# Optimization experiments

Hardware: AMD Instinct MI355X
Metric: run time of the kernel (lower is better)

## Reference

```python
import jax, jax.numpy as jnp
import numpy as np

N = 50000
E = 1600000
D = 128
H = 16  # SE hidden = int(128 * 0.125)
EPS = 1e-5


def _layernorm(x, gamma, beta):
    mu = jnp.mean(x, axis=-1, keepdims=True)
    var = jnp.mean(jnp.square(x - mu), axis=-1, keepdims=True)
    return (x - mu) * jax.lax.rsqrt(var + EPS) * gamma + beta


def _gcn_conv(x, W, b, src, dst):
    # PyG GCNConv, improved=True: self-loop weight 2.0, symmetric norm.
    xw = x @ W                                        # [N, D]
    deg = jax.ops.segment_sum(jnp.ones((E,), x.dtype), dst, num_segments=N) + 2.0
    dinv = jnp.where(deg > 0, jax.lax.rsqrt(deg), 0.0)  # [N]
    norm = dinv[src] * dinv[dst]                      # [E]
    agg = jax.ops.segment_sum(xw[src] * norm[:, None], dst, num_segments=N)
    agg = agg + xw * (2.0 * dinv * dinv)[:, None]     # self-loop contribution
    return agg + b


def setup_inputs() -> dict:
    key = jax.random.key(0)
    ks = jax.random.split(key, 10)
    scale = 1.0 / np.sqrt(D)
    inp = {
        "x": jax.random.normal(ks[0], (N, D), jnp.float32),
        "edge_index": jax.random.randint(ks[1], (2, E), 0, N, jnp.int64),
        "W1": jax.random.normal(ks[2], (D, D), jnp.float32) * scale,
        "b1": jnp.zeros((D,), jnp.float32),
        "g1": jnp.ones((D,), jnp.float32),
        "beta1": jnp.zeros((D,), jnp.float32),
        "W2": jax.random.normal(ks[3], (D, D), jnp.float32) * scale,
        "b2": jnp.zeros((D,), jnp.float32),
        "g2": jnp.ones((D,), jnp.float32),
        "beta2": jnp.zeros((D,), jnp.float32),
        "Ws": jax.random.normal(ks[4], (D, H), jnp.float32) * scale,
        "bs": jnp.zeros((H,), jnp.float32),
        "We": jax.random.normal(ks[5], (H, D), jnp.float32) * (1.0 / np.sqrt(H)),
        "be": jnp.zeros((D,), jnp.float32),
    }
    return inp


def reference(x, edge_index, W1, b1, g1, beta1, W2, b2, g2, beta2, Ws, bs, We, be):
    src, dst = edge_index[0], edge_index[1]
    skip = x
    h = jax.nn.relu(_layernorm(_gcn_conv(x, W1, b1, src, dst), g1, beta1))
    h = _layernorm(_gcn_conv(h, W2, b2, src, dst), g2, beta2)
    # SE gating
    s = jax.nn.relu(h @ Ws + bs)
    w = jax.nn.sigmoid(s @ We + be)
    h = h * w
    return jax.nn.relu(h + skip)
```

## Files before the change

kernel.cpp:

```cpp
#include <hip/hip_runtime.h>
#include <math.h>

#define DD 128
#define HH 16
#define NB 256
#define TILE 8192
#define SEGCAP 24576
#define EPSV 1e-5f

typedef unsigned long long u64;

static __device__ __forceinline__ ushort f2bf(float f) {
  uint u = __float_as_uint(f);
  u += 0x7FFFu + ((u >> 16) & 1u);
  return (ushort)(u >> 16);
}
static __device__ __forceinline__ float bflo(uint u) { return __uint_as_float(u << 16); }
static __device__ __forceinline__ float bfhi(uint u) { return __uint_as_float(u & 0xFFFF0000u); }


__global__ void k_hist(const int* __restrict__ dst, int* __restrict__ deg, int ecnt) {
  int stride = gridDim.x * blockDim.x;
  for (int e = blockIdx.x * blockDim.x + threadIdx.x; e < ecnt; e += stride)
    atomicAdd(&deg[dst[e]], 1);
}


#define SCAN_T 1024
#define SCAN_I 4

__global__ void k_scan1(const int* __restrict__ deg, u64* __restrict__ bsum, int n) {
  __shared__ u64 sh[SCAN_T];
  int tid = threadIdx.x;
  int base = blockIdx.x * SCAN_T * SCAN_I + tid * SCAN_I;
  u64 s = 0;
#pragma unroll
  for (int j = 0; j < SCAN_I; ++j) {
    int i = base + j;
    if (i < n) {
      int d = deg[i];
      int dp = (d + 7) & ~7;
      s += ((u64)dp << 32) | (u64)(uint)d;
    }
  }
  sh[tid] = s;
  __syncthreads();
  for (int off = SCAN_T / 2; off > 0; off >>= 1) {
    if (tid < off) sh[tid] += sh[tid + off];
    __syncthreads();
  }
  if (tid == 0) bsum[blockIdx.x] = sh[0];
}

__global__ void k_scan2(const int* __restrict__ deg, const u64* __restrict__ bsum,
                        int* __restrict__ rowoff, int* __restrict__ cursor,
                        int* __restrict__ bucketBase, int* __restrict__ bucketCur,
                        int n) {
  __shared__ u64 sh[SCAN_T];
  __shared__ u64 sbase;
  int tid = threadIdx.x;
  int b = blockIdx.x;
  if (tid == 0) { u64 s = 0; for (int j = 0; j < b; ++j) s += bsum[j]; sbase = s; }
  int base = b * SCAN_T * SCAN_I + tid * SCAN_I;
  int d[SCAN_I]; u64 ts = 0;
#pragma unroll
  for (int j = 0; j < SCAN_I; ++j) {
    int i = base + j;
    d[j] = (i < n) ? deg[i] : 0;
    int dp = (d[j] + 7) & ~7;
    ts += ((u64)dp << 32) | (u64)(uint)d[j];
  }
  sh[tid] = ts;
  __syncthreads();
  for (int off = 1; off < SCAN_T; off <<= 1) {
    u64 v = (tid >= off) ? sh[tid - off] : 0;
    __syncthreads();
    sh[tid] += v;
    __syncthreads();
  }
  u64 ex = sbase + sh[tid] - ts;
#pragma unroll
  for (int j = 0; j < SCAN_I; ++j) {
    int i = base + j;
    if (i < n) {
      int ro = (int)(ex >> 32);
      int raw = (int)(ex & 0xFFFFFFFFu);
      rowoff[i] = ro;
      cursor[i] = ro;
      int bq = (int)(((uint)i * NB) / (uint)n);
      if (i == (bq * n + NB - 1) / NB) { bucketBase[bq] = raw; bucketCur[bq] = raw; }
      int dp = (d[j] + 7) & ~7;
      ex += ((u64)dp << 32) | (u64)(uint)d[j];
      if (i == n - 1) rowoff[n] = (int)(ex >> 32);
    }
  }
}


static __device__ __forceinline__ void gemm_f32_body(
    const float* __restrict__ A, const float* __restrict__ B,
    const int* __restrict__ deg, ushort* __restrict__ C, int nrows, int bx,
    float* Bs) {
  int tid = threadIdx.x;
  int tx = tid & 15, ty = tid >> 4;
  int rowbase = (bx >> 1) * 128;
  int c0 = (bx & 1) * 64;
  {
    int kk = tid >> 4;
    int cc = (tid & 15) * 4;
#pragma unroll
    for (int p = 0; p < 8; ++p) {
      int k = p * 16 + kk;
      float4 bv = *reinterpret_cast<const float4*>(&B[k * DD + c0 + cc]);
      *reinterpret_cast<float4*>(&Bs[k * 64 + cc]) = bv;
    }
  }
  __syncthreads();
  float acc[8][4];
#pragma unroll
  for (int i = 0; i < 8; ++i)
#pragma unroll
    for (int j = 0; j < 4; ++j) acc[i][j] = 0.f;
  int rl[8];
#pragma unroll
  for (int i = 0; i < 8; ++i) {
    int r = rowbase + ty * 8 + i;
    rl[i] = (r < nrows) ? r : (nrows - 1);
  }
  const float4* A4 = reinterpret_cast<const float4*>(A);
  for (int kq = 0; kq < 32; ++kq) {
    float4 av[8];
#pragma unroll
    for (int i = 0; i < 8; ++i) av[i] = A4[(size_t)rl[i] * 32 + kq];
#pragma unroll
    for (int j = 0; j < 4; ++j) {
      float4 bv = *reinterpret_cast<const float4*>(&Bs[(kq * 4 + j) * 64 + tx * 4]);
#pragma unroll
      for (int i = 0; i < 8; ++i) {
        float a = (j == 0) ? av[i].x : (j == 1) ? av[i].y : (j == 2) ? av[i].z : av[i].w;
        acc[i][0] = fmaf(a, bv.x, acc[i][0]);
        acc[i][1] = fmaf(a, bv.y, acc[i][1]);
        acc[i][2] = fmaf(a, bv.z, acc[i][2]);
        acc[i][3] = fmaf(a, bv.w, acc[i][3]);
      }
    }
  }
  int cbase = c0 + tx * 4;
#pragma unroll
  for (int i = 0; i < 8; ++i) {
    int r = rowbase + ty * 8 + i;
    if (r < nrows) {
      float dv = rsqrtf((float)deg[r] + 2.0f);
      ushort4 o;
      o.x = f2bf(acc[i][0] * dv); o.y = f2bf(acc[i][1] * dv);
      o.z = f2bf(acc[i][2] * dv); o.w = f2bf(acc[i][3] * dv);
      *reinterpret_cast<ushort4*>(&C[(size_t)r * DD + cbase]) = o;
    }
  }
}


__global__ __launch_bounds__(256) void k_gemm1_bucket(
    const float* __restrict__ A, const float* __restrict__ B,
    const int* __restrict__ deg, ushort* __restrict__ C, int nrows,
    const int* __restrict__ src, const int* __restrict__ dst,
    int* __restrict__ bucketCur, uint* __restrict__ pairs, int ecnt,
    int abloks, int gblocks) {
  __shared__ uint smem[8960];
  int bx = blockIdx.x;
  if (bx >= abloks) {
    gemm_f32_body(A, B, deg, C, nrows, bx - abloks, (float*)smem);
    return;
  }
  uint* stag  = smem;
  uint* cnt   = smem + 8192;
  uint* gbase = smem + 8448;
  uint* cur   = smem + 8704;
  int tid = threadIdx.x;
  int ntiles = (ecnt + TILE - 1) / TILE;
  for (int t = bx; t < ntiles; t += abloks) {
    int base = t * TILE;
    int cntE = min(TILE, ecnt - base);
    cnt[tid] = 0;
    __syncthreads();
    for (int k = tid; k < cntE; k += 256) {
      uint d = (uint)dst[base + k];
      atomicAdd(&cnt[(d * NB) / (uint)nrows], 1u);
    }
    __syncthreads();
    uint myc = cnt[tid];
    uint gb = atomicAdd((uint*)&bucketCur[tid], myc);
    uint v = myc;
#pragma unroll
    for (int off = 1; off < 64; off <<= 1) {
      uint u = __shfl_up(v, off, 64);
      if ((tid & 63) >= off) v += u;
    }
    if ((tid & 63) == 63) gbase[tid >> 6] = v;
    __syncthreads();
    uint add = 0;
#pragma unroll
    for (int wvi = 0; wvi < 4; ++wvi) add += (wvi < (tid >> 6)) ? gbase[wvi] : 0;
    uint excl = add + v - myc;
    __syncthreads();
    cnt[tid] = excl;
    gbase[tid] = gb;
    cur[tid] = 0;
    __syncthreads();
    for (int k = tid; k < cntE; k += 256) {
      uint d = (uint)dst[base + k];
      uint s = (uint)src[base + k];
      uint b = (d * NB) / (uint)nrows;
      uint li = atomicAdd(&cur[b], 1u);
      stag[cnt[b] + li] = (d << 16) | s;
    }
    __syncthreads();
    int wv = tid >> 6, ln = tid & 63;
    for (int b = wv; b < 256; b += 4) {
      uint c = cur[b], o = cnt[b], g = gbase[b];
      for (uint k2 = (uint)ln; k2 < c; k2 += 64) pairs[g + k2] = stag[o + k2];
    }
    __syncthreads();
  }
}


__global__ __launch_bounds__(256) void k_csrb(
    const uint* __restrict__ pairs, const int* __restrict__ bucketBase,
    const int* __restrict__ rowoff, const int* __restrict__ deg,
    int* __restrict__ cursor, ushort* __restrict__ csr, int n, int ecnt) {
  __shared__ ushort seg[SEGCAP];
  __shared__ int curs[256];
  int b = blockIdx.x;
  int tid = threadIdx.x;
  int d0 = (b * n + NB - 1) / NB;
  int d1 = ((b + 1) * n + NB - 1) / NB;
  int segbase = rowoff[d0];
  int seglen = rowoff[d1] - segbase;
  int pbase = bucketBase[b];
  int pend = (b == NB - 1) ? ecnt : bucketBase[b + 1];
  if (seglen <= SEGCAP) {
    for (int dl = tid; dl < d1 - d0; dl += 256) curs[dl] = rowoff[d0 + dl] - segbase;
    __syncthreads();
    for (int p = pbase + tid; p < pend; p += 256) {
      uint pr = pairs[p];
      int pos = atomicAdd(&curs[(int)(pr >> 16) - d0], 1);
      seg[pos] = (ushort)(pr & 0xFFFFu);
    }
    __syncthreads();
    for (int dl = tid; dl < d1 - d0; dl += 256) {
      int e0 = curs[dl], e1 = rowoff[d0 + dl + 1] - segbase;
      for (int k = e0; k < e1; ++k) seg[k] = (ushort)n;
    }
    __syncthreads();
    uint4* outp4 = (uint4*)(csr + segbase);
    const uint4* sp = (const uint4*)seg;
    int nq = seglen >> 3;
    for (int k = tid; k < nq; k += 256) outp4[k] = sp[k];
  } else {
    for (int p = pbase + tid; p < pend; p += 256) {
      uint pr = pairs[p];
      int pos = atomicAdd(&cursor[pr >> 16], 1);
      csr[pos] = (ushort)(pr & 0xFFFFu);
    }
    __syncthreads();
    for (int dl = tid; dl < d1 - d0; dl += 256) {
      int d = d0 + dl;
      for (int k = rowoff[d] + deg[d]; k < rowoff[d + 1]; ++k) csr[k] = (ushort)n;
    }
  }
}


__global__ __launch_bounds__(256) void k_gemmb(const ushort* __restrict__ A,
                                               const float* __restrict__ B,
                                               const int* __restrict__ deg,
                                               ushort* __restrict__ C, int nrows) {
  __shared__ float Bs[DD * 64];
  int tid = threadIdx.x;
  int tx = tid & 15, ty = tid >> 4;
  int rowbase = (blockIdx.x >> 1) * 128;
  int c0 = (blockIdx.x & 1) * 64;
  {
    int kk = tid >> 4;
    int cc = (tid & 15) * 4;
#pragma unroll
    for (int p = 0; p < 8; ++p) {
      int k = p * 16 + kk;
      float4 bv = *reinterpret_cast<const float4*>(&B[k * DD + c0 + cc]);
      *reinterpret_cast<float4*>(&Bs[k * 64 + cc]) = bv;
    }
  }
  __syncthreads();
  float acc[8][4];
#pragma unroll
  for (int i = 0; i < 8; ++i)
#pragma unroll
    for (int j = 0; j < 4; ++j) acc[i][j] = 0.f;
  int rl[8];
#pragma unroll
  for (int i = 0; i < 8; ++i) {
    int r = rowbase + ty * 8 + i;
    rl[i] = (r < nrows) ? r : (nrows - 1);
  }
  const uint4* A16 = reinterpret_cast<const uint4*>(A);
  for (int kq = 0; kq < 16; ++kq) {
    uint4 av[8];
#pragma unroll
    for (int i = 0; i < 8; ++i) av[i] = A16[(size_t)rl[i] * 16 + kq];
#pragma unroll
    for (int kk = 0; kk < 8; ++kk) {
      float4 bv = *reinterpret_cast<const float4*>(&Bs[(kq * 8 + kk) * 64 + tx * 4]);
#pragma unroll
      for (int i = 0; i < 8; ++i) {
        uint wq = (kk < 2) ? av[i].x : (kk < 4) ? av[i].y : (kk < 6) ? av[i].z : av[i].w;
        float a = (kk & 1) ? bfhi(wq) : bflo(wq);
        acc[i][0] = fmaf(a, bv.x, acc[i][0]);
        acc[i][1] = fmaf(a, bv.y, acc[i][1]);
        acc[i][2] = fmaf(a, bv.z, acc[i][2]);
        acc[i][3] = fmaf(a, bv.w, acc[i][3]);
      }
    }
  }
  int cbase = c0 + tx * 4;
#pragma unroll
  for (int i = 0; i < 8; ++i) {
    int r = rowbase + ty * 8 + i;
    if (r < nrows) {
      float dv = rsqrtf((float)deg[r] + 2.0f);
      ushort4 o;
      o.x = f2bf(acc[i][0] * dv); o.y = f2bf(acc[i][1] * dv);
      o.z = f2bf(acc[i][2] * dv); o.w = f2bf(acc[i][3] * dv);
      *reinterpret_cast<ushort4*>(&C[(size_t)r * DD + cbase]) = o;
    }
  }
}


static __device__ __forceinline__ void edge_accum(
    const uint* __restrict__ xw32, const ushort* __restrict__ csr,
    int start, int cnt, uint lane, float& acc0, float& acc1) {
  const uint4* cs = (const uint4*)(csr + __builtin_amdgcn_readfirstlane(start));
  int rem = __builtin_amdgcn_readfirstlane(cnt);
  uint4 c;
  if (rem >= 8) c = *cs++;
  while (rem >= 16) {
    uint v[8];
    v[0] = xw32[((c.x & 0xFFFFu) << 6) + lane];
    v[1] = xw32[((c.x >> 16) << 6) + lane];
    v[2] = xw32[((c.y & 0xFFFFu) << 6) + lane];
    v[3] = xw32[((c.y >> 16) << 6) + lane];
    v[4] = xw32[((c.z & 0xFFFFu) << 6) + lane];
    v[5] = xw32[((c.z >> 16) << 6) + lane];
    v[6] = xw32[((c.w & 0xFFFFu) << 6) + lane];
    v[7] = xw32[((c.w >> 16) << 6) + lane];
    uint4 cn = *cs++;
#pragma unroll
    for (int j = 0; j < 8; ++j) {
      acc0 += bflo(v[j]);
      acc1 += bfhi(v[j]);
    }
    c = cn; rem -= 8;
  }
  if (rem >= 8) {
    uint v[8];
    v[0] = xw32[((c.x & 0xFFFFu) << 6) + lane];
    v[1] = xw32[((c.x >> 16) << 6) + lane];
    v[2] = xw32[((c.y & 0xFFFFu) << 6) + lane];
    v[3] = xw32[((c.y >> 16) << 6) + lane];
    v[4] = xw32[((c.z & 0xFFFFu) << 6) + lane];
    v[5] = xw32[((c.z >> 16) << 6) + lane];
    v[6] = xw32[((c.w & 0xFFFFu) << 6) + lane];
    v[7] = xw32[((c.w >> 16) << 6) + lane];
#pragma unroll
    for (int j = 0; j < 8; ++j) {
      acc0 += bflo(v[j]);
      acc1 += bfhi(v[j]);
    }
  }
}


__global__ __launch_bounds__(256) void k_agg1(
    const ushort* __restrict__ xwd, const ushort* __restrict__ csr,
    const int* __restrict__ rowoff, const int* __restrict__ deg,
    const float* __restrict__ bias, const float* __restrict__ gam,
    const float* __restrict__ bet, uint* __restrict__ outp, int n) {
  int wv = threadIdx.x >> 6, lane = threadIdx.x & 63;
  int i = blockIdx.x * 4 + wv;
  if (i >= n) return;
  int start = rowoff[i], cnt = rowoff[i + 1] - start;
  float di = rsqrtf((float)deg[i] + 2.0f);
  const uint* xw32 = (const uint*)xwd;
  float acc0 = 0.f, acc1 = 0.f;
  edge_accum(xw32, csr, start, cnt, (uint)lane, acc0, acc1);
  uint su = xw32[((uint)i << 6) + lane];
  float2 bv = ((const float2*)bias)[lane];
  float c0v = fmaf(di, acc0 + 2.f * bflo(su), bv.x);
  float c1v = fmaf(di, acc1 + 2.f * bfhi(su), bv.y);
  float s = c0v + c1v;
#pragma unroll
  for (int off = 32; off > 0; off >>= 1) s += __shfl_xor(s, off);
  float mu = s * (1.f / DD);
  float c0 = c0v - mu, c1 = c1v - mu;
  float q = c0 * c0 + c1 * c1;
#pragma unroll
  for (int off = 32; off > 0; off >>= 1) q += __shfl_xor(q, off);
  float rstd = rsqrtf(q * (1.f / DD) + EPSV);
  float2 gv = ((const float2*)gam)[lane];
  float2 tv = ((const float2*)bet)[lane];
  float h0 = fmaxf(fmaf(c0 * rstd, gv.x, tv.x), 0.f);
  float h1 = fmaxf(fmaf(c1 * rstd, gv.y, tv.y), 0.f);
  uint packed = (uint)f2bf(h0) | ((uint)f2bf(h1) << 16);
  __builtin_nontemporal_store(packed, &outp[((uint)i << 6) + lane]);
}


__global__ __launch_bounds__(256) void k_agg2(
    const ushort* __restrict__ xwd, const ushort* __restrict__ csr,
    const int* __restrict__ rowoff, const int* __restrict__ deg,
    const float* __restrict__ bias, const float* __restrict__ gam,
    const float* __restrict__ bet, const float* __restrict__ Ws,
    const float* __restrict__ bs, const float* __restrict__ We,
    const float* __restrict__ be, const float* __restrict__ xin,
    float* __restrict__ outp, int n) {
  int wv = threadIdx.x >> 6, lane = threadIdx.x & 63;
  int i = blockIdx.x * 4 + wv;
  if (i >= n) return;
  int start = rowoff[i], cnt = rowoff[i + 1] - start;
  float di = rsqrtf((float)deg[i] + 2.0f);
  const uint* xw32 = (const uint*)xwd;
  float acc0 = 0.f, acc1 = 0.f;
  edge_accum(xw32, csr, start, cnt, (uint)lane, acc0, acc1);
  uint su = xw32[((uint)i << 6) + lane];
  float2 bv = ((const float2*)bias)[lane];
  float c0v = fmaf(di, acc0 + 2.f * bflo(su), bv.x);
  float c1v = fmaf(di, acc1 + 2.f * bfhi(su), bv.y);
  float s = c0v + c1v;
#pragma unroll
  for (int off = 32; off > 0; off >>= 1) s += __shfl_xor(s, off);
  float mu = s * (1.f / DD);
  float c0 = c0v - mu, c1 = c1v - mu;
  float q = c0 * c0 + c1 * c1;
#pragma unroll
  for (int off = 32; off > 0; off >>= 1) q += __shfl_xor(q, off);
  float rstd = rsqrtf(q * (1.f / DD) + EPSV);
  float2 gv = ((const float2*)gam)[lane];
  float2 tv = ((const float2*)bet)[lane];
  float h0 = fmaf(c0 * rstd, gv.x, tv.x);
  float h1 = fmaf(c1 * rstd, gv.y, tv.y);
  float pj[HH];
  const float* wr0 = &Ws[(2 * lane) * HH];
  const float* wr1 = &Ws[(2 * lane + 1) * HH];
#pragma unroll
  for (int j = 0; j < HH; ++j) pj[j] = h0 * wr0[j] + h1 * wr1[j];
#pragma unroll
  for (int off = 32; off > 0; off >>= 1) {
#pragma unroll
    for (int j = 0; j < HH; ++j) pj[j] += __shfl_xor(pj[j], off);
  }
  float2 bev = ((const float2*)be)[lane];
  float wacc0 = bev.x, wacc1 = bev.y;
#pragma unroll
  for (int j = 0; j < HH; ++j) {
    float sj = fmaxf(pj[j] + bs[j], 0.f);
    float2 wev = ((const float2*)(We + j * DD))[lane];
    wacc0 = fmaf(sj, wev.x, wacc0);
    wacc1 = fmaf(sj, wev.y, wacc1);
  }
  float w0 = 1.f / (1.f + __expf(-wacc0));
  float w1 = 1.f / (1.f + __expf(-wacc1));
  float2 xr = ((const float2*)(xin + (size_t)i * DD))[lane];
  float2 o;
  o.x = fmaxf(fmaf(h0, w0, xr.x), 0.f);
  o.y = fmaxf(fmaf(h1, w1, xr.y), 0.f);
  ((float2*)(outp + (size_t)i * DD))[lane] = o;
}


extern "C" void kernel_launch(void* const* d_in, const int* in_sizes, int n_in,
                              void* d_out, int out_size, void* d_ws, size_t ws_size,
                              hipStream_t stream) {
  const float* x   = (const float*)d_in[0];
  const int*   ei  = (const int*)d_in[1];
  const float* W1  = (const float*)d_in[2];
  const float* b1  = (const float*)d_in[3];
  const float* g1  = (const float*)d_in[4];
  const float* be1 = (const float*)d_in[5];
  const float* W2  = (const float*)d_in[6];
  const float* b2  = (const float*)d_in[7];
  const float* g2  = (const float*)d_in[8];
  const float* be2 = (const float*)d_in[9];
  const float* Ws  = (const float*)d_in[10];
  const float* bs  = (const float*)d_in[11];
  const float* We  = (const float*)d_in[12];
  const float* bee = (const float*)d_in[13];
  float* outp = (float*)d_out;

  int n    = in_sizes[0] / DD;
  int ecnt = in_sizes[1] / 2;
  const int* src = ei;
  const int* dst = ei + ecnt;

  size_t maxent = (size_t)ecnt + 8 * (size_t)n + 64;

  char* w = (char*)d_ws;
  ushort* xwd    = (ushort*)w; w += (size_t)(n + 1) * DD * 2;
  uint*   h1     = (uint*)w;   w += (size_t)n * DD * 2;
  int*    deg    = (int*)w;    w += (size_t)n * 4;
  int*    cursor = (int*)w;    w += (size_t)n * 4;
  int*    rowoff = (int*)w;    w += (size_t)(n + 1) * 4;
  w = (char*)(((size_t)w + 7) & ~(size_t)7);
  u64*    bsum   = (u64*)w;    w += 64 * 8;
  int*    bktB   = (int*)w;    w += NB * 4;
  int*    bktC   = (int*)w;    w += NB * 4;
  w = (char*)(((size_t)w + 15) & ~(size_t)15);
  uint*   pairs  = (uint*)w;   w += ((size_t)ecnt + 64) * 4;
  w = (char*)(((size_t)w + 15) & ~(size_t)15);
  ushort* csr    = (ushort*)w; w += maxent * 2;

  hipMemsetAsync(deg, 0, (size_t)n * 4, stream);
  hipMemsetAsync(xwd + (size_t)n * DD, 0, DD * 2, stream);

  const int TB = 256;
  k_hist<<<2048, TB, 0, stream>>>(dst, deg, ecnt);
  int nb = (n + SCAN_T * SCAN_I - 1) / (SCAN_T * SCAN_I);
  k_scan1<<<nb, SCAN_T, 0, stream>>>(deg, bsum, n);
  k_scan2<<<nb, SCAN_T, 0, stream>>>(deg, bsum, rowoff, cursor, bktB, bktC, n);

  int gblocks = ((n + 127) / 128) * 2;
  int abloks = (ecnt + TILE - 1) / TILE;
  k_gemm1_bucket<<<abloks + gblocks, TB, 0, stream>>>(
      x, W1, deg, xwd, n, src, dst, bktC, pairs, ecnt, abloks, gblocks);
  k_csrb<<<NB, TB, 0, stream>>>(pairs, bktB, rowoff, deg, cursor, csr, n, ecnt);

  int nb4 = (n + 3) / 4;
  k_agg1<<<nb4, TB, 0, stream>>>(xwd, csr, rowoff, deg, b1, g1, be1, h1, n);
  k_gemmb<<<gblocks, TB, 0, stream>>>((const ushort*)h1, W2, deg, xwd, n);
  k_agg2<<<nb4, TB, 0, stream>>>(xwd, csr, rowoff, deg, b2, g2, be2,
                                 Ws, bs, We, bee, x, outp, n);
}
```

Before: 326.7 us.

## Use bf16 MFMA for both dense GEMMs, pre-converting x to bf16 in histogram

Replaces the FP32 scalar-FMA GEMM bodies for XW1 and H1·W2 with a bf16 MFMA 16x16x32 kernel. Each wave loads its B fragments straight from global memory and converts them to bf16, with no LDS staging. The input x is converted to bf16 inside the degree-histogram kernel so the first GEMM can read packed bf16 rows, which costs an extra workspace buffer and a pass over x. This lowers first-layer GEMM precision to bf16 inputs, and output stores become 2-byte scattered writes per lane rather than vectorized.

Result: faster. 310.9 us (-4.8%).

```diff
diff --git a/kernel.cpp b/kernel.cpp
--- a/kernel.cpp
+++ b/kernel.cpp
@@ -9,6 +9,9 @@
 #define EPSV 1e-5f
 
 typedef unsigned long long u64;
+typedef __attribute__((ext_vector_type(8))) short short8;
+typedef __attribute__((ext_vector_type(4))) float f32x4;
+union U4S8 { uint4 u; short8 s; };
 
 static __device__ __forceinline__ ushort f2bf(float f) {
   uint u = __float_as_uint(f);
@@ -19,10 +22,16 @@
 static __device__ __forceinline__ float bfhi(uint u) { return __uint_as_float(u & 0xFFFF0000u); }
 
 
-__global__ void k_hist(const int* __restrict__ dst, int* __restrict__ deg, int ecnt) {
+__global__ void k_hist_cvt(const int* __restrict__ dst, int* __restrict__ deg, int ecnt,
+                           const float2* __restrict__ x2, uint* __restrict__ xb,
+                           int ncnt) {
   int stride = gridDim.x * blockDim.x;
-  for (int e = blockIdx.x * blockDim.x + threadIdx.x; e < ecnt; e += stride)
-    atomicAdd(&deg[dst[e]], 1);
+  int t0 = blockIdx.x * blockDim.x + threadIdx.x;
+  for (int e = t0; e < ecnt; e += stride) atomicAdd(&deg[dst[e]], 1);
+  for (int k = t0; k < ncnt; k += stride) {
+    float2 v = x2[k];
+    xb[k] = (uint)f2bf(v.x) | ((uint)f2bf(v.y) << 16);
+  }
 }
 
 
@@ -97,71 +106,52 @@
 }
 
 
-static __device__ __forceinline__ void gemm_f32_body(
-    const float* __restrict__ A, const float* __restrict__ B,
-    const int* __restrict__ deg, ushort* __restrict__ C, int nrows, int bx,
-    float* Bs) {
+static __device__ __forceinline__ void gemm_mfma_body(
+    const uint4* __restrict__ A16, const float* __restrict__ B,
+    const int* __restrict__ deg, ushort* __restrict__ C, int nrows, int bx) {
   int tid = threadIdx.x;
-  int tx = tid & 15, ty = tid >> 4;
-  int rowbase = (bx >> 1) * 128;
+  int wv = tid >> 6, l = tid & 63;
+  int rowbase = (bx >> 1) * 64;
   int c0 = (bx & 1) * 64;
-  {
-    int kk = tid >> 4;
-    int cc = (tid & 15) * 4;
-#pragma unroll
-    for (int p = 0; p < 8; ++p) {
-      int k = p * 16 + kk;
-      float4 bv = *reinterpret_cast<const float4*>(&B[k * DD + c0 + cc]);
-      *reinterpret_cast<float4*>(&Bs[k * 64 + cc]) = bv;
-    }
-  }
-  __syncthreads();
-  float acc[8][4];
-#pragma unroll
-  for (int i = 0; i < 8; ++i)
-#pragma unroll
-    for (int j = 0; j < 4; ++j) acc[i][j] = 0.f;
-  int rl[8];
-#pragma unroll
-  for (int i = 0; i < 8; ++i) {
-    int r = rowbase + ty * 8 + i;
-    rl[i] = (r < nrows) ? r : (nrows - 1);
-  }
-  const float4* A4 = reinterpret_cast<const float4*>(A);
-  for (int kq = 0; kq < 32; ++kq) {
-    float4 av[8];
-#pragma unroll
-    for (int i = 0; i < 8; ++i) av[i] = A4[(size_t)rl[i] * 32 + kq];
-#pragma unroll
-    for (int j = 0; j < 4; ++j) {
-      float4 bv = *reinterpret_cast<const float4*>(&Bs[(kq * 4 + j) * 64 + tx * 4]);
-#pragma unroll
-      for (int i = 0; i < 8; ++i) {
-        float a = (j == 0) ? av[i].x : (j == 1) ? av[i].y : (j == 2) ? av[i].z : av[i].w;
-        acc[i][0] = fmaf(a, bv.x, acc[i][0]);
-        acc[i][1] = fmaf(a, bv.y, acc[i][1]);
-        acc[i][2] = fmaf(a, bv.z, acc[i][2]);
-        acc[i][3] = fmaf(a, bv.w, acc[i][3]);
+  int colb = c0 + (wv << 4) + (l & 15);
+  int kb = (l >> 4) << 3;
+  uint4 bf[4];
+#pragma unroll
+  for (int ks = 0; ks < 4; ++ks) {
+    const float* Bp = B + (size_t)(ks * 32 + kb) * DD + colb;
+    float b0 = Bp[0], b1 = Bp[DD], b2 = Bp[2 * DD], b3 = Bp[3 * DD];
+    float b4 = Bp[4 * DD], b5 = Bp[5 * DD], b6 = Bp[6 * DD], b7 = Bp[7 * DD];
+    bf[ks].x = (uint)f2bf(b0) | ((uint)f2bf(b1) << 16);
+    bf[ks].y = (uint)f2bf(b2) | ((uint)f2bf(b3) << 16);
+    bf[ks].z = (uint)f2bf(b4) | ((uint)f2bf(b5) << 16);
+    bf[ks].w = (uint)f2bf(b6) | ((uint)f2bf(b7) << 16);
+  }
+#pragma unroll
+  for (int rt = 0; rt < 4; ++rt) {
+    int r = rowbase + rt * 16 + (l & 15);
+    int rc = (r < nrows) ? r : (nrows - 1);
+    f32x4 acc = {0.f, 0.f, 0.f, 0.f};
+#pragma unroll
+    for (int ks = 0; ks < 4; ++ks) {
+      U4S8 ua, ub;
+      ua.u = A16[(size_t)rc * 16 + (ks << 2) + (l >> 4)];
+      ub.u = bf[ks];
+      acc = __builtin_amdgcn_mfma_f32_16x16x32_bf16(ua.s, ub.s, acc, 0, 0, 0);
+    }
+#pragma unroll
+    for (int ri = 0; ri < 4; ++ri) {
+      int row = rowbase + rt * 16 + ((l >> 4) << 2) + ri;
+      if (row < nrows) {
+        float dv = rsqrtf((float)deg[row] + 2.0f);
+        C[(size_t)row * DD + colb] = f2bf(acc[ri] * dv);
       }
     }
   }
-  int cbase = c0 + tx * 4;
-#pragma unroll
-  for (int i = 0; i < 8; ++i) {
-    int r = rowbase + ty * 8 + i;
-    if (r < nrows) {
-      float dv = rsqrtf((float)deg[r] + 2.0f);
-      ushort4 o;
-      o.x = f2bf(acc[i][0] * dv); o.y = f2bf(acc[i][1] * dv);
-      o.z = f2bf(acc[i][2] * dv); o.w = f2bf(acc[i][3] * dv);
-      *reinterpret_cast<ushort4*>(&C[(size_t)r * DD + cbase]) = o;
-    }
-  }
 }
 
 
 __global__ __launch_bounds__(256) void k_gemm1_bucket(
-    const float* __restrict__ A, const float* __restrict__ B,
+    const uint4* __restrict__ A16, const float* __restrict__ B,
     const int* __restrict__ deg, ushort* __restrict__ C, int nrows,
     const int* __restrict__ src, const int* __restrict__ dst,
     int* __restrict__ bucketCur, uint* __restrict__ pairs, int ecnt,
@@ -169,7 +159,7 @@
   __shared__ uint smem[8960];
   int bx = blockIdx.x;
   if (bx >= abloks) {
-    gemm_f32_body(A, B, deg, C, nrows, bx - abloks, (float*)smem);
+    gemm_mfma_body(A16, B, deg, C, nrows, bx - abloks);
     return;
   }
   uint* stag  = smem;
@@ -222,6 +212,12 @@
     }
     __syncthreads();
   }
+}
+
+__global__ __launch_bounds__(256) void k_gemmb(
+    const uint4* __restrict__ A16, const float* __restrict__ B,
+    const int* __restrict__ deg, ushort* __restrict__ C, int nrows) {
+  gemm_mfma_body(A16, B, deg, C, nrows, blockIdx.x);
 }
 
 
@@ -267,71 +263,6 @@
     for (int dl = tid; dl < d1 - d0; dl += 256) {
       int d = d0 + dl;
       for (int k = rowoff[d] + deg[d]; k < rowoff[d + 1]; ++k) csr[k] = (ushort)n;
-    }
-  }
-}
-
-
-__global__ __launch_bounds__(256) void k_gemmb(const ushort* __restrict__ A,
-                                               const float* __restrict__ B,
-                                               const int* __restrict__ deg,
-                                               ushort* __restrict__ C, int nrows) {
-  __shared__ float Bs[DD * 64];
-  int tid = threadIdx.x;
-  int tx = tid & 15, ty = tid >> 4;
-  int rowbase = (blockIdx.x >> 1) * 128;
-  int c0 = (blockIdx.x & 1) * 64;
-  {
-    int kk = tid >> 4;
-    int cc = (tid & 15) * 4;
-#pragma unroll
-    for (int p = 0; p < 8; ++p) {
-      int k = p * 16 + kk;
-      float4 bv = *reinterpret_cast<const float4*>(&B[k * DD + c0 + cc]);
-      *reinterpret_cast<float4*>(&Bs[k * 64 + cc]) = bv;
-    }
-  }
-  __syncthreads();
-  float acc[8][4];
-#pragma unroll
-  for (int i = 0; i < 8; ++i)
-#pragma unroll
-    for (int j = 0; j < 4; ++j) acc[i][j] = 0.f;
-  int rl[8];
-#pragma unroll
-  for (int i = 0; i < 8; ++i) {
-    int r = rowbase + ty * 8 + i;
-    rl[i] = (r < nrows) ? r : (nrows - 1);
-  }
-  const uint4* A16 = reinterpret_cast<const uint4*>(A);
-  for (int kq = 0; kq < 16; ++kq) {
-    uint4 av[8];
-#pragma unroll
-    for (int i = 0; i < 8; ++i) av[i] = A16[(size_t)rl[i] * 16 + kq];
-#pragma unroll
-    for (int kk = 0; kk < 8; ++kk) {
-      float4 bv = *reinterpret_cast<const float4*>(&Bs[(kq * 8 + kk) * 64 + tx * 4]);
-#pragma unroll
-      for (int i = 0; i < 8; ++i) {
-        uint wq = (kk < 2) ? av[i].x : (kk < 4) ? av[i].y : (kk < 6) ? av[i].z : av[i].w;
-        float a = (kk & 1) ? bfhi(wq) : bflo(wq);
-        acc[i][0] = fmaf(a, bv.x, acc[i][0]);
-        acc[i][1] = fmaf(a, bv.y, acc[i][1]);
-        acc[i][2] = fmaf(a, bv.z, acc[i][2]);
-        acc[i][3] = fmaf(a, bv.w, acc[i][3]);
-      }
-    }
-  }
-  int cbase = c0 + tx * 4;
-#pragma unroll
-  for (int i = 0; i < 8; ++i) {
-    int r = rowbase + ty * 8 + i;
-    if (r < nrows) {
-      float dv = rsqrtf((float)deg[r] + 2.0f);
-      ushort4 o;
-      o.x = f2bf(acc[i][0] * dv); o.y = f2bf(acc[i][1] * dv);
-      o.z = f2bf(acc[i][2] * dv); o.w = f2bf(acc[i][3] * dv);
-      *reinterpret_cast<ushort4*>(&C[(size_t)r * DD + cbase]) = o;
     }
   }
 }
@@ -507,6 +438,7 @@
   char* w = (char*)d_ws;
   ushort* xwd    = (ushort*)w; w += (size_t)(n + 1) * DD * 2;
   uint*   h1     = (uint*)w;   w += (size_t)n * DD * 2;
+  uint*   xb     = (uint*)w;   w += (size_t)n * DD * 2;
   int*    deg    = (int*)w;    w += (size_t)n * 4;
   int*    cursor = (int*)w;    w += (size_t)n * 4;
   int*    rowoff = (int*)w;    w += (size_t)(n + 1) * 4;
@@ -523,20 +455,20 @@
   hipMemsetAsync(xwd + (size_t)n * DD, 0, DD * 2, stream);
 
   const int TB = 256;
-  k_hist<<<2048, TB, 0, stream>>>(dst, deg, ecnt);
+  k_hist_cvt<<<2048, TB, 0, stream>>>(dst, deg, ecnt, (const float2*)x, xb, n * 64);
   int nb = (n + SCAN_T * SCAN_I - 1) / (SCAN_T * SCAN_I);
   k_scan1<<<nb, SCAN_T, 0, stream>>>(deg, bsum, n);
   k_scan2<<<nb, SCAN_T, 0, stream>>>(deg, bsum, rowoff, cursor, bktB, bktC, n);
 
-  int gblocks = ((n + 127) / 128) * 2;
+  int gblocks = ((n + 63) / 64) * 2;
   int abloks = (ecnt + TILE - 1) / TILE;
   k_gemm1_bucket<<<abloks + gblocks, TB, 0, stream>>>(
-      x, W1, deg, xwd, n, src, dst, bktC, pairs, ecnt, abloks, gblocks);
+      (const uint4*)xb, W1, deg, xwd, n, src, dst, bktC, pairs, ecnt, abloks, gblocks);
   k_csrb<<<NB, TB, 0, stream>>>(pairs, bktB, rowoff, deg, cursor, csr, n, ecnt);
 
   int nb4 = (n + 3) / 4;
   k_agg1<<<nb4, TB, 0, stream>>>(xwd, csr, rowoff, deg, b1, g1, be1, h1, n);
-  k_gemmb<<<gblocks, TB, 0, stream>>>((const ushort*)h1, W2, deg, xwd, n);
+  k_gemmb<<<gblocks, TB, 0, stream>>>((const uint4*)h1, W2, deg, xwd, n);
   k_agg2<<<nb4, TB, 0, stream>>>(xwd, csr, rowoff, deg, b2, g2, be2,
                                  Ws, bs, We, bee, x, outp, n);
 }
```
